# Kernel optimization log

Measured on AMD Instinct MI355X. Metric: run time of the kernel, lower is better.

## Reference

```python
import jax, jax.numpy as jnp
import numpy as np

B, OBS, GENC, H, C, NF = 16384, 512, 216, 1024, 64, 8
IN = GENC + OBS + OBS  # use_state=True: [graph, state, next_state]


def setup_inputs() -> dict:
    key = jax.random.key(0)
    ks = jax.random.split(key, 9)
    graph = jax.random.randint(ks[0], (B, GENC), 0, 2).astype(jnp.float32)
    state = jax.random.normal(ks[1], (B, OBS), dtype=jnp.float32)
    next_state = jax.random.normal(ks[2], (B, OBS), dtype=jnp.float32)
    W1 = jax.random.normal(ks[3], (NF, IN, H), dtype=jnp.float32) * 0.02
    b1 = jnp.zeros((NF, H), dtype=jnp.float32)
    W2 = jax.random.normal(ks[4], (NF, H, H), dtype=jnp.float32) * 0.02
    b2 = jnp.zeros((NF, H), dtype=jnp.float32)
    W3 = jax.random.normal(ks[5], (NF, H, C), dtype=jnp.float32) * 0.02
    b3 = jnp.zeros((NF, C), dtype=jnp.float32)
    return {"graph": graph, "state": state, "next_state": next_state,
            "W1": W1, "b1": b1, "W2": W2, "b2": b2, "W3": W3, "b3": b3}


def reference(graph, state, next_state, W1, b1, W2, b2, W3, b3):
    # wide_diayn forward: concat input, run per-factor MLP on rows where
    # graph[:, i] == 1, later factors overwrite earlier; unmatched rows -> 0.
    x = jnp.concatenate([graph, state, next_state], axis=-1)  # [B, IN]
    nf = W1.shape[0]
    mask = graph[:, :nf] == 1.0  # [B, F] per-factor indicator
    h = jax.nn.relu(jnp.einsum('bi,fih->bfh', x, W1) + b1[None, :, :])
    h = jax.nn.relu(jnp.einsum('bfh,fhg->bfg', h, W2) + b2[None, :, :])
    out_all = jnp.einsum('bfg,fgc->bfc', h, W3) + b3[None, :, :]  # [B, F, C]
    rev_first = jnp.argmax(mask[:, ::-1].astype(jnp.int32), axis=1)
    last_idx = (nf - 1) - rev_first  # [B]
    sel = jnp.take_along_axis(out_all, last_idx[:, None, None], axis=1)[:, 0, :]
    any_active = mask.any(axis=1)
    return jnp.where(any_active[:, None], sel, jnp.zeros_like(sel))
```

## Files before the change

kernel.cpp:

```cpp
#include <hip/hip_runtime.h>

#define BB   16384
#define GENC 216
#define OBS  512
#define NH   1024
#define NC   64
#define NFAC 8
#define NIN  1240
#define KP1  1280
#define MTILES 136

typedef __attribute__((ext_vector_type(4))) float f32x4;
typedef __attribute__((ext_vector_type(8))) short short8;
typedef __attribute__((ext_vector_type(4))) short short4v;

__device__ __forceinline__ unsigned short f2bf(float f) {
  union { float f; unsigned u; } x; x.f = f;
  unsigned r = x.u + 0x7fffu + ((x.u >> 16) & 1u);
  return (unsigned short)(r >> 16);
}

__device__ __forceinline__ void gl_lds16(const unsigned short* g, unsigned short* l) {
  __builtin_amdgcn_global_load_lds(
      (const __attribute__((address_space(1))) void*)g,
      (__attribute__((address_space(3))) void*)l, 16, 0, 0);
}

__device__ __forceinline__ int xcd_chunk(int gid, int nwg) {
  int q = nwg >> 3, r = nwg & 7, x = gid & 7, p = gid >> 3;
  return (x < r ? x * (q + 1) : r * (q + 1) + (x - r) * q) + p;
}

__global__ void bucket_kernel(const float* __restrict__ graph,
                              int* __restrict__ cnt, int* __restrict__ rowlist) {
  __shared__ int lcnt[NFAC];
  __shared__ int lbase[NFAC];
  int tid = threadIdx.x;
  if (tid < NFAC) lcnt[tid] = 0;
  __syncthreads();
  int b = blockIdx.x * 256 + tid;
  const float* g = graph + (size_t)b * GENC;
  float4 g0 = *(const float4*)g;
  float4 g1 = *(const float4*)(g + 4);
  int f = -1;
  if (g0.x == 1.f) f = 0;
  if (g0.y == 1.f) f = 1;
  if (g0.z == 1.f) f = 2;
  if (g0.w == 1.f) f = 3;
  if (g1.x == 1.f) f = 4;
  if (g1.y == 1.f) f = 5;
  if (g1.z == 1.f) f = 6;
  if (g1.w == 1.f) f = 7;
  int li = 0;
  if (f >= 0) li = atomicAdd(&lcnt[f], 1);
  __syncthreads();
  if (tid < NFAC) lbase[tid] = lcnt[tid] ? atomicAdd(&cnt[tid], lcnt[tid]) : 0;
  __syncthreads();
  if (f >= 0) rowlist[f * BB + lbase[f] + li] = b;
}

__global__ void gather_x(const float* __restrict__ graph,
                         const float* __restrict__ state,
                         const float* __restrict__ nexts,
                         const int* __restrict__ cnt,
                         const int* __restrict__ rowlist,
                         unsigned short* __restrict__ xg) {
  int w = threadIdx.x >> 6, lane = threadIdx.x & 63;
  int pos = blockIdx.x * 4 + w;
  int f = -1, loc = 0, acc = 0;
#pragma unroll
  for (int i = 0; i < NFAC; ++i) {
    int c = cnt[i];
    if (f < 0 && pos < acc + c) { f = i; loc = pos - acc; }
    acc += c;
  }
  if (f < 0) return;
  int b = rowlist[f * BB + loc];
  unsigned short* dst = xg + (size_t)pos * KP1;
#pragma unroll
  for (int it = 0; it < 5; ++it) {
    int c = it * 64 + lane;
    float4 v;
    if (c < 54)       v = *(const float4*)(graph + (size_t)b * GENC + c * 4);
    else if (c < 182) v = *(const float4*)(state + (size_t)b * OBS + (c - 54) * 4);
    else if (c < 310) v = *(const float4*)(nexts + (size_t)b * OBS + (c - 182) * 4);
    else              v = make_float4(0.f, 0.f, 0.f, 0.f);
    short4v s;
    s[0] = (short)f2bf(v.x); s[1] = (short)f2bf(v.y);
    s[2] = (short)f2bf(v.z); s[3] = (short)f2bf(v.w);
    *(short4v*)(dst + c * 4) = s;
  }
}

__global__ void transpose_all(const float* __restrict__ W1,
                              const float* __restrict__ W2,
                              const float* __restrict__ W3,
                              unsigned short* __restrict__ w1t,
                              unsigned short* __restrict__ w2t,
                              unsigned short* __restrict__ w3t) {
  __shared__ unsigned short tile[64][65];
  int z = blockIdx.z;
  const float* src; unsigned short* dst; int K, N, KPad;
  if (z < 8)        { src = W1 + (size_t)z * NIN * NH;       dst = w1t + (size_t)z * NH * KP1; K = NIN; N = NH; KPad = KP1; }
  else if (z < 16)  { src = W2 + (size_t)(z - 8) * NH * NH;  dst = w2t + (size_t)(z - 8) * NH * NH; K = NH; N = NH; KPad = NH; }
  else              { src = W3 + (size_t)(z - 16) * NH * NC; dst = w3t + (size_t)(z - 16) * NC * NH; K = NH; N = NC; KPad = NH; }
  int k0 = blockIdx.y * 64, n0 = blockIdx.x * 64;
  if (k0 >= KPad || n0 >= N) return;
  int tr = threadIdx.x >> 6, tc = threadIdx.x & 63;
#pragma unroll
  for (int i = 0; i < 16; ++i) {
    int r = i * 4 + tr;
    int k = k0 + r;
    float v = (k < K) ? src[(size_t)k * N + n0 + tc] : 0.0f;
    tile[r][tc] = f2bf(v);
  }
  __syncthreads();
  int kp = threadIdx.x & 31, nb = threadIdx.x >> 5;
#pragma unroll
  for (int i = 0; i < 8; ++i) {
    int n = i * 8 + nb;
    union { short2 s2; unsigned u; } v;
    v.s2.x = (short)tile[kp * 2][n];
    v.s2.y = (short)tile[kp * 2 + 1][n];
    *(unsigned*)(dst + (size_t)(n0 + n) * KPad + k0 + kp * 2) = v.u;
  }
}

template <int LAYER>
__launch_bounds__(256, 2)
__global__ void mlp_gemm(const unsigned short* __restrict__ Abase,
                         const unsigned short* __restrict__ Wt,
                         const float* __restrict__ bias,
                         unsigned short* __restrict__ Hout,
                         float* __restrict__ Out,
                         const int* __restrict__ cnt,
                         const int* __restrict__ rowlist) {
  constexpr int N  = (LAYER == 3) ? NC : NH;
  constexpr int K  = (LAYER == 1) ? KP1 : NH;
  constexpr int BM = 128;
  constexpr int BN = (LAYER == 3) ? 64 : 128;
  constexpr int NB = (LAYER == 3) ? 1 : (NH / 128);
  constexpr int NKT = K / 64;
  constexpr int MF = (LAYER == 3) ? 2 : 4;
  constexpr int BI = (LAYER == 3) ? 2 : 4;

  const int wg = xcd_chunk(blockIdx.x, MTILES * NB);
  const int ty = wg / NB;
  const int n0 = (wg % NB) * BN;

  int f = -1, m0 = 0, goff = 0, cntf = 0;
  {
    int acc = 0, off = 0;
#pragma unroll
    for (int i = 0; i < NFAC; ++i) {
      int c = cnt[i];
      int t = (c + BM - 1) >> 7;
      if (f < 0 && ty < acc + t) { f = i; m0 = (ty - acc) * BM; goff = off; cntf = c; }
      acc += t; off += c;
    }
  }
  if (f < 0) return;

  __shared__ unsigned short As[2][BM * 64];
  __shared__ unsigned short Bs[2][BN * 64];

  const int tid = threadIdx.x;
  const int wid = tid >> 6, lane = tid & 63;
  const int wm = (LAYER == 3) ? wid : (wid >> 1);
  const int wn = (LAYER == 3) ? 0 : (wid & 1);

  const int rl = lane >> 3;
  const int chs = (lane & 7) ^ rl;
  const unsigned short* pA[4];
  const unsigned short* pB[BI];
  {
    const unsigned short* Aorg = Abase + (size_t)(goff + m0) * K;
    const unsigned short* Borg = Wt + (size_t)f * N * K + (size_t)n0 * K;
#pragma unroll
    for (int i = 0; i < 4; ++i)
      pA[i] = Aorg + (size_t)(wid * 32 + i * 8 + rl) * K + chs * 8;
#pragma unroll
    for (int i = 0; i < BI; ++i)
      pB[i] = Borg + (size_t)(wid * (8 * BI) + i * 8 + rl) * K + chs * 8;
  }

  f32x4 acc[MF][4];
#pragma unroll
  for (int a = 0; a < MF; ++a)
#pragma unroll
    for (int b = 0; b < 4; ++b) acc[a][b] = (f32x4){0.f, 0.f, 0.f, 0.f};

  auto stage = [&](int buf) {
#pragma unroll
    for (int i = 0; i < 4; ++i) {
      gl_lds16(pA[i], &As[buf][(wid * 32 + i * 8) * 64]);
      pA[i] += 64;
    }
#pragma unroll
    for (int i = 0; i < BI; ++i) {
      gl_lds16(pB[i], &Bs[buf][(wid * (8 * BI) + i * 8) * 64]);
      pB[i] += 64;
    }
  };

  auto compute = [&](int buf) {
#pragma unroll
    for (int ks = 0; ks < 2; ++ks) {
      const int kc8 = ks * 4 + (lane >> 4);
      short8 av[MF], bv[4];
#pragma unroll
      for (int mf = 0; mf < MF; ++mf) {
        int row = wm * (MF * 16) + mf * 16 + (lane & 15);
        av[mf] = *(const short8*)(&As[buf][0] + row * 64 + ((kc8 ^ (row & 7)) << 3));
      }
#pragma unroll
      for (int nf = 0; nf < 4; ++nf) {
        int col = wn * 64 + nf * 16 + (lane & 15);
        bv[nf] = *(const short8*)(&Bs[buf][0] + col * 64 + ((kc8 ^ (col & 7)) << 3));
      }
      __builtin_amdgcn_s_setprio(1);
#pragma unroll
      for (int mf = 0; mf < MF; ++mf)
#pragma unroll
        for (int nf = 0; nf < 4; ++nf)
          acc[mf][nf] = __builtin_amdgcn_mfma_f32_16x16x32_bf16(
              av[mf], bv[nf], acc[mf][nf], 0, 0, 0);
      __builtin_amdgcn_s_setprio(0);
    }
  };

  stage(0);
  stage(1);
#pragma unroll 1
  for (int kt = 0; kt < NKT; ++kt) {
    if (kt < NKT - 1) {
      if constexpr (LAYER == 3)
        asm volatile("s_waitcnt vmcnt(6)" ::: "memory");
      else
        asm volatile("s_waitcnt vmcnt(8)" ::: "memory");
    } else {
      asm volatile("s_waitcnt vmcnt(0)" ::: "memory");
    }
    __builtin_amdgcn_sched_barrier(0);
    __builtin_amdgcn_s_barrier();
    __builtin_amdgcn_sched_barrier(0);
    compute(kt & 1);
    __builtin_amdgcn_sched_barrier(0);
    __builtin_amdgcn_s_barrier();
    __builtin_amdgcn_sched_barrier(0);
    if (kt + 2 < NKT) stage(kt & 1);
  }

  if (LAYER == 3) {
    const float* bs = bias + f * NC;
#pragma unroll
    for (int nf = 0; nf < 4; ++nf) {
      int col = nf * 16 + (lane & 15);
      float bv = bs[col];
#pragma unroll
      for (int mf = 0; mf < MF; ++mf) {
        int rbase = wm * (MF * 16) + mf * 16 + ((lane >> 4) << 2);
#pragma unroll
        for (int i = 0; i < 4; ++i) {
          int pos = m0 + rbase + i;
          if (pos < cntf) {
            int b = rowlist[f * BB + pos];
            Out[(size_t)b * NC + col] = acc[mf][nf][i] + bv;
          }
        }
      }
    }
  } else {
    const float* bs = bias + f * NH;
#pragma unroll
    for (int nf = 0; nf < 4; ++nf) {
      int col = n0 + wn * 64 + nf * 16 + (lane & 15);
      float bv = bs[col];
#pragma unroll
      for (int mf = 0; mf < MF; ++mf) {
        int rbase = wm * (MF * 16) + mf * 16 + ((lane >> 4) << 2);
#pragma unroll
        for (int i = 0; i < 4; ++i) {
          int pos = m0 + rbase + i;
          if (pos < cntf) {
            float v = fmaxf(acc[mf][nf][i] + bv, 0.0f);
            Hout[(size_t)(goff + pos) * NH + col] = f2bf(v);
          }
        }
      }
    }
  }
}

extern "C" void kernel_launch(void* const* d_in, const int* in_sizes, int n_in,
                              void* d_out, int out_size, void* d_ws, size_t ws_size,
                              hipStream_t stream) {
  const float* graph = (const float*)d_in[0];
  const float* state = (const float*)d_in[1];
  const float* nexts = (const float*)d_in[2];
  const float* W1 = (const float*)d_in[3];
  const float* b1 = (const float*)d_in[4];
  const float* W2 = (const float*)d_in[5];
  const float* b2 = (const float*)d_in[6];
  const float* W3 = (const float*)d_in[7];
  const float* b3 = (const float*)d_in[8];
  float* out = (float*)d_out;
  char* ws = (char*)d_ws;

  const size_t ROWCAP = BB + 128;
  const size_t OFF_ROW = 256;
  const size_t OFF_W1T = OFF_ROW + (size_t)NFAC * BB * 4;
  const size_t OFF_W2T = OFF_W1T + (size_t)NFAC * NH * KP1 * 2;
  const size_t OFF_W3T = OFF_W2T + (size_t)NFAC * NH * NH * 2;
  const size_t OFF_H1  = OFF_W3T + (size_t)NFAC * NC * NH * 2;
  const size_t OFF_XG  = OFF_H1 + ROWCAP * NH * 2;

  int* cnt = (int*)ws;
  int* rowlist = (int*)(ws + OFF_ROW);
  unsigned short* w1t = (unsigned short*)(ws + OFF_W1T);
  unsigned short* w2t = (unsigned short*)(ws + OFF_W2T);
  unsigned short* w3t = (unsigned short*)(ws + OFF_W3T);
  unsigned short* h1  = (unsigned short*)(ws + OFF_H1);
  unsigned short* xg  = (unsigned short*)(ws + OFF_XG);
  unsigned short* h2  = xg;

  hipMemsetAsync(cnt, 0, 64, stream);
  hipMemsetAsync(d_out, 0, (size_t)out_size * sizeof(float), stream);

  bucket_kernel<<<BB / 256, 256, 0, stream>>>(graph, cnt, rowlist);
  gather_x<<<BB / 4, 256, 0, stream>>>(graph, state, nexts, cnt, rowlist, xg);
  transpose_all<<<dim3(16, 20, 24), 256, 0, stream>>>(W1, W2, W3, w1t, w2t, w3t);

  mlp_gemm<1><<<MTILES * (NH / 128), 256, 0, stream>>>(
      xg, w1t, b1, h1, nullptr, cnt, rowlist);
  mlp_gemm<2><<<MTILES * (NH / 128), 256, 0, stream>>>(
      h1, w2t, b2, h2, nullptr, cnt, rowlist);
  mlp_gemm<3><<<MTILES, 256, 0, stream>>>(
      h2, w3t, b3, nullptr, out, cnt, rowlist);
}
```

Measured before the change: 254.0 us.

## Use 256x256-tile 512-thread GEMM kernel for first two MLP layers

Adds a new GEMM kernel with 256x256 output tiles, 8 waves, 128KB double-buffered LDS with async global-to-LDS loads, split-phase staging and setprio around MFMA blocks. Layers 1 and 2 now use it, with the grid derived from per-factor row counts rounded up to 256. The larger tile raises arithmetic intensity and operand reuse from LDS, but gives fewer workgroups and more padding waste per factor bucket, plus higher register and LDS pressure. The workspace row cap is enlarged to cover the 256-row padding.

```diff
diff --git a/kernel.cpp b/kernel.cpp
--- a/kernel.cpp
+++ b/kernel.cpp
@@ -9,6 +9,7 @@
 #define NIN  1240
 #define KP1  1280
 #define MTILES 136
+#define MT256  72
 
 typedef __attribute__((ext_vector_type(4))) float f32x4;
 typedef __attribute__((ext_vector_type(8))) short short8;
@@ -127,6 +128,172 @@
 }
 
 template <int LAYER>
+__launch_bounds__(512, 2)
+__global__ void mlp_gemm256(const unsigned short* __restrict__ Abase,
+                            const unsigned short* __restrict__ Wt,
+                            const float* __restrict__ bias,
+                            unsigned short* __restrict__ Hout,
+                            const int* __restrict__ cnt) {
+  constexpr int K  = (LAYER == 1) ? KP1 : NH;
+  constexpr int NT = K / 64;
+  constexpr int NB = NH / 256;
+
+  extern __shared__ unsigned short smem[];
+  unsigned short* As0 = smem;
+  unsigned short* As1 = smem + 16384;
+  unsigned short* Bs0 = smem + 32768;
+  unsigned short* Bs1 = smem + 49152;
+
+  const int wg = xcd_chunk(blockIdx.x, MT256 * NB);
+  const int ty = wg / NB;
+  const int n0 = (wg % NB) * 256;
+
+  int f = -1, m0 = 0, goff = 0, cntf = 0;
+  {
+    int acc = 0, off = 0;
+#pragma unroll
+    for (int i = 0; i < NFAC; ++i) {
+      int c = cnt[i];
+      int t = (c + 255) >> 8;
+      if (f < 0 && ty < acc + t) { f = i; m0 = (ty - acc) * 256; goff = off; cntf = c; }
+      acc += t; off += c;
+    }
+  }
+  if (f < 0) return;
+
+  const int tid = threadIdx.x, wid = tid >> 6, lane = tid & 63;
+  const int wm = wid >> 2, wn = wid & 3;
+
+  const int sr = tid >> 3;
+  const int sc = (tid & 7) ^ (sr & 7);
+  const unsigned short* pu[8];
+  {
+    const unsigned short* Ao = Abase + (size_t)(goff + m0) * K;
+    const unsigned short* Bo = Wt + (size_t)f * NH * K + (size_t)n0 * K;
+#pragma unroll
+    for (int u = 0; u < 4; ++u) pu[u] = Ao + (size_t)(u * 64 + sr) * K + sc * 8;
+#pragma unroll
+    for (int u = 0; u < 4; ++u) pu[4 + u] = Bo + (size_t)(u * 64 + sr) * K + sc * 8;
+  }
+  const int ldst = wid * 512;
+
+  f32x4 acc[8][4];
+#pragma unroll
+  for (int a = 0; a < 8; ++a)
+#pragma unroll
+    for (int b = 0; b < 4; ++b) acc[a][b] = (f32x4){0.f, 0.f, 0.f, 0.f};
+
+  auto stage6 = [&](unsigned short* Ab, unsigned short* Bb) {
+    gl_lds16(pu[0], Ab + 0 * 4096 + ldst); pu[0] += 64;
+    gl_lds16(pu[2], Ab + 2 * 4096 + ldst); pu[2] += 64;
+#pragma unroll
+    for (int u = 0; u < 4; ++u) { gl_lds16(pu[4 + u], Bb + u * 4096 + ldst); pu[4 + u] += 64; }
+  };
+  auto stage2 = [&](unsigned short* Ab) {
+    gl_lds16(pu[1], Ab + 1 * 4096 + ldst); pu[1] += 64;
+    gl_lds16(pu[3], Ab + 3 * 4096 + ldst); pu[3] += 64;
+  };
+
+  short8 bfr[4][2];
+
+  stage6(As0, Bs0);
+  stage2(As0);
+
+#pragma unroll 1
+  for (int t = 0; t < NT; ++t) {
+    unsigned short* Ab = (t & 1) ? As1 : As0;
+    unsigned short* Bb = (t & 1) ? Bs1 : Bs0;
+    unsigned short* An = (t & 1) ? As0 : As1;
+    unsigned short* Bn = (t & 1) ? Bs0 : Bs1;
+
+    asm volatile("s_waitcnt vmcnt(2)" ::: "memory");
+    __builtin_amdgcn_sched_barrier(0);
+    __builtin_amdgcn_s_barrier();
+    __builtin_amdgcn_sched_barrier(0);
+    {
+      short8 afr[4][2];
+#pragma unroll
+      for (int nf = 0; nf < 4; ++nf) {
+        int c = wn * 64 + nf * 16 + (lane & 15);
+#pragma unroll
+        for (int ks = 0; ks < 2; ++ks) {
+          int kc = ks * 4 + (lane >> 4);
+          bfr[nf][ks] = *(const short8*)(Bb + c * 64 + ((kc ^ (c & 7)) << 3));
+        }
+      }
+#pragma unroll
+      for (int mf = 0; mf < 4; ++mf) {
+        int r = wm * 128 + mf * 16 + (lane & 15);
+#pragma unroll
+        for (int ks = 0; ks < 2; ++ks) {
+          int kc = ks * 4 + (lane >> 4);
+          afr[mf][ks] = *(const short8*)(Ab + r * 64 + ((kc ^ (r & 7)) << 3));
+        }
+      }
+      if (t + 1 < NT) stage6(An, Bn);
+      __builtin_amdgcn_s_setprio(1);
+#pragma unroll
+      for (int mf = 0; mf < 4; ++mf)
+#pragma unroll
+        for (int nf = 0; nf < 4; ++nf)
+#pragma unroll
+          for (int ks = 0; ks < 2; ++ks)
+            acc[mf][nf] = __builtin_amdgcn_mfma_f32_16x16x32_bf16(
+                afr[mf][ks], bfr[nf][ks], acc[mf][nf], 0, 0, 0);
+      __builtin_amdgcn_s_setprio(0);
+    }
+
+    if (t + 1 < NT) { asm volatile("s_waitcnt vmcnt(6)" ::: "memory"); }
+    else            { asm volatile("s_waitcnt vmcnt(0)" ::: "memory"); }
+    __builtin_amdgcn_sched_barrier(0);
+    __builtin_amdgcn_s_barrier();
+    __builtin_amdgcn_sched_barrier(0);
+    {
+      short8 afr[4][2];
+#pragma unroll
+      for (int mf = 0; mf < 4; ++mf) {
+        int r = wm * 128 + (mf + 4) * 16 + (lane & 15);
+#pragma unroll
+        for (int ks = 0; ks < 2; ++ks) {
+          int kc = ks * 4 + (lane >> 4);
+          afr[mf][ks] = *(const short8*)(Ab + r * 64 + ((kc ^ (r & 7)) << 3));
+        }
+      }
+      if (t + 1 < NT) stage2(An);
+      __builtin_amdgcn_s_setprio(1);
+#pragma unroll
+      for (int mf = 0; mf < 4; ++mf)
+#pragma unroll
+        for (int nf = 0; nf < 4; ++nf)
+#pragma unroll
+          for (int ks = 0; ks < 2; ++ks)
+            acc[mf + 4][nf] = __builtin_amdgcn_mfma_f32_16x16x32_bf16(
+                afr[mf][ks], bfr[nf][ks], acc[mf + 4][nf], 0, 0, 0);
+      __builtin_amdgcn_s_setprio(0);
+    }
+  }
+
+  const float* bs = bias + f * NH;
+#pragma unroll
+  for (int nf = 0; nf < 4; ++nf) {
+    int col = n0 + wn * 64 + nf * 16 + (lane & 15);
+    float bv = bs[col];
+#pragma unroll
+    for (int mf = 0; mf < 8; ++mf) {
+      int rbase = wm * 128 + mf * 16 + ((lane >> 4) << 2);
+#pragma unroll
+      for (int i = 0; i < 4; ++i) {
+        int pos = m0 + rbase + i;
+        if (pos < cntf) {
+          float v = fmaxf(acc[mf][nf][i] + bv, 0.0f);
+          Hout[(size_t)(goff + pos) * NH + col] = f2bf(v);
+        }
+      }
+    }
+  }
+}
+
+template <int LAYER>
 __launch_bounds__(256, 2)
 __global__ void mlp_gemm(const unsigned short* __restrict__ Abase,
                          const unsigned short* __restrict__ Wt,
@@ -307,7 +474,7 @@
   float* out = (float*)d_out;
   char* ws = (char*)d_ws;
 
-  const size_t ROWCAP = BB + 128;
+  const size_t ROWCAP = BB + 256;
   const size_t OFF_ROW = 256;
   const size_t OFF_W1T = OFF_ROW + (size_t)NFAC * BB * 4;
   const size_t OFF_W2T = OFF_W1T + (size_t)NFAC * NH * KP1 * 2;
@@ -324,6 +491,11 @@
   unsigned short* xg  = (unsigned short*)(ws + OFF_XG);
   unsigned short* h2  = xg;
 
+  hipFuncSetAttribute(reinterpret_cast<const void*>(mlp_gemm256<1>),
+                      hipFuncAttributeMaxDynamicSharedMemorySize, 131072);
+  hipFuncSetAttribute(reinterpret_cast<const void*>(mlp_gemm256<2>),
+                      hipFuncAttributeMaxDynamicSharedMemorySize, 131072);
+
   hipMemsetAsync(cnt, 0, 64, stream);
   hipMemsetAsync(d_out, 0, (size_t)out_size * sizeof(float), stream);
 
@@ -331,10 +503,7 @@
   gather_x<<<BB / 4, 256, 0, stream>>>(graph, state, nexts, cnt, rowlist, xg);
   transpose_all<<<dim3(16, 20, 24), 256, 0, stream>>>(W1, W2, W3, w1t, w2t, w3t);
 
-  mlp_gemm<1><<<MTILES * (NH / 128), 256, 0, stream>>>(
-      xg, w1t, b1, h1, nullptr, cnt, rowlist);
-  mlp_gemm<2><<<MTILES * (NH / 128), 256, 0, stream>>>(
-      h1, w2t, b2, h2, nullptr, cnt, rowlist);
-  mlp_gemm<3><<<MTILES, 256, 0, stream>>>(
-      h2, w3t, b3, nullptr, out, cnt, rowlist);
-}
+  mlp_gemm256<1><<<MT256 * 4, 512, 131072, stream>>>(xg, w1t, b1, h1, cnt);
+  mlp_gemm256<2><<<MT256 * 4, 512, 131072, stream>>>(h1, w2t, b2, h2, cnt);
+  mlp_gemm<3><<<MTILES, 256, 0, stream>>>(h2, w3t, b3, nullptr, out, cnt, rowlist);
+}
```

After: 270.1 us. +6.3%, slower.

## Use 128x256 tiles with 8 waves and triple-buffered LDS for hidden GEMMs

Applied to the files above, without the earlier changes.

Layers 1 and 2 move to a new kernel that computes 128x256 output tiles with 512 threads and three LDS buffers in dynamic shared memory. The next stage's global-to-LDS loads are issued after the fragment reads but before the MFMAs, so copies overlap the math. The wider N tile raises the ratio of MFMA work to loaded data and halves the number of A-tile reloads. The cost is large LDS use (about 144 KB), which likely limits each CU to one workgroup. The output layer is split into its own unchanged kernel.

```diff
diff --git a/kernel.cpp b/kernel.cpp
--- a/kernel.cpp
+++ b/kernel.cpp
@@ -127,26 +127,21 @@
 }
 
 template <int LAYER>
-__launch_bounds__(256, 2)
-__global__ void mlp_gemm(const unsigned short* __restrict__ Abase,
-                         const unsigned short* __restrict__ Wt,
-                         const float* __restrict__ bias,
-                         unsigned short* __restrict__ Hout,
-                         float* __restrict__ Out,
-                         const int* __restrict__ cnt,
-                         const int* __restrict__ rowlist) {
-  constexpr int N  = (LAYER == 3) ? NC : NH;
+__launch_bounds__(512, 2)
+__global__ void mlp_gemm_big(const unsigned short* __restrict__ Abase,
+                             const unsigned short* __restrict__ Wt,
+                             const float* __restrict__ bias,
+                             unsigned short* __restrict__ Hout,
+                             const int* __restrict__ cnt) {
   constexpr int K  = (LAYER == 1) ? KP1 : NH;
-  constexpr int BM = 128;
-  constexpr int BN = (LAYER == 3) ? 64 : 128;
-  constexpr int NB = (LAYER == 3) ? 1 : (NH / 128);
-  constexpr int NKT = K / 64;
-  constexpr int MF = (LAYER == 3) ? 2 : 4;
-  constexpr int BI = (LAYER == 3) ? 2 : 4;
+  constexpr int NT = K / 64;
+  constexpr int NB = NH / 256;
+
+  extern __shared__ unsigned short smem[];
 
   const int wg = xcd_chunk(blockIdx.x, MTILES * NB);
   const int ty = wg / NB;
-  const int n0 = (wg % NB) * BN;
+  const int n0 = (wg % NB) * 256;
 
   int f = -1, m0 = 0, goff = 0, cntf = 0;
   {
@@ -154,39 +149,162 @@
 #pragma unroll
     for (int i = 0; i < NFAC; ++i) {
       int c = cnt[i];
-      int t = (c + BM - 1) >> 7;
-      if (f < 0 && ty < acc + t) { f = i; m0 = (ty - acc) * BM; goff = off; cntf = c; }
+      int t = (c + 127) >> 7;
+      if (f < 0 && ty < acc + t) { f = i; m0 = (ty - acc) * 128; goff = off; cntf = c; }
       acc += t; off += c;
     }
   }
   if (f < 0) return;
 
-  __shared__ unsigned short As[2][BM * 64];
-  __shared__ unsigned short Bs[2][BN * 64];
+  const int tid = threadIdx.x, wid = tid >> 6, lane = tid & 63;
+  const int wm = wid >> 2, wn = wid & 3;
+
+  const int sr = tid >> 3;
+  const int sc = (tid & 7) ^ (sr & 7);
+  const unsigned short* pu[6];
+  {
+    const unsigned short* Ao = Abase + (size_t)(goff + m0) * K;
+    const unsigned short* Bo = Wt + (size_t)f * NH * K + (size_t)n0 * K;
+    pu[0] = Ao + (size_t)sr * K + sc * 8;
+    pu[1] = Ao + (size_t)(64 + sr) * K + sc * 8;
+#pragma unroll
+    for (int u = 0; u < 4; ++u) pu[2 + u] = Bo + (size_t)(u * 64 + sr) * K + sc * 8;
+  }
+  const int dst8 = tid * 8;
+
+  unsigned short* A0 = smem;              unsigned short* B0 = smem + 8192;
+  unsigned short* A1 = smem + 24576;      unsigned short* B1 = A1 + 8192;
+  unsigned short* A2 = smem + 49152;      unsigned short* B2 = A2 + 8192;
+
+  f32x4 acc[4][4];
+#pragma unroll
+  for (int a = 0; a < 4; ++a)
+#pragma unroll
+    for (int b = 0; b < 4; ++b) acc[a][b] = (f32x4){0.f, 0.f, 0.f, 0.f};
+
+  auto stage = [&](unsigned short* Ab, unsigned short* Bb) {
+    gl_lds16(pu[0], Ab + dst8);        pu[0] += 64;
+    gl_lds16(pu[1], Ab + 4096 + dst8); pu[1] += 64;
+#pragma unroll
+    for (int u = 0; u < 4; ++u) { gl_lds16(pu[2 + u], Bb + u * 4096 + dst8); pu[2 + u] += 64; }
+  };
+
+  stage(A0, B0);
+  stage(A1, B1);
+  unsigned short *Ac = A0, *Bc = B0, *An = A1, *Bn = B1, *Af = A2, *Bf = B2;
+
+#pragma unroll 1
+  for (int t = 0; t < NT; ++t) {
+    if (t < NT - 1) { asm volatile("s_waitcnt vmcnt(6)" ::: "memory"); }
+    else            { asm volatile("s_waitcnt vmcnt(0)" ::: "memory"); }
+    __builtin_amdgcn_sched_barrier(0);
+    __builtin_amdgcn_s_barrier();
+    __builtin_amdgcn_sched_barrier(0);
+
+    short8 av[4][2], bv[4][2];
+#pragma unroll
+    for (int nf = 0; nf < 4; ++nf) {
+      int c = wn * 64 + nf * 16 + (lane & 15);
+#pragma unroll
+      for (int ks = 0; ks < 2; ++ks) {
+        int kc = ks * 4 + (lane >> 4);
+        bv[nf][ks] = *(const short8*)(Bc + c * 64 + ((kc ^ (c & 7)) << 3));
+      }
+    }
+#pragma unroll
+    for (int mf = 0; mf < 4; ++mf) {
+      int r = wm * 64 + mf * 16 + (lane & 15);
+#pragma unroll
+      for (int ks = 0; ks < 2; ++ks) {
+        int kc = ks * 4 + (lane >> 4);
+        av[mf][ks] = *(const short8*)(Ac + r * 64 + ((kc ^ (r & 7)) << 3));
+      }
+    }
+    if (t + 2 < NT) stage(Af, Bf);
+    __builtin_amdgcn_s_setprio(1);
+#pragma unroll
+    for (int mf = 0; mf < 4; ++mf)
+#pragma unroll
+      for (int nf = 0; nf < 4; ++nf)
+#pragma unroll
+        for (int ks = 0; ks < 2; ++ks)
+          acc[mf][nf] = __builtin_amdgcn_mfma_f32_16x16x32_bf16(
+              av[mf][ks], bv[nf][ks], acc[mf][nf], 0, 0, 0);
+    __builtin_amdgcn_s_setprio(0);
+    unsigned short* ta = Ac; unsigned short* tb = Bc;
+    Ac = An; Bc = Bn; An = Af; Bn = Bf; Af = ta; Bf = tb;
+  }
+
+  const float* bs = bias + f * NH;
+#pragma unroll
+  for (int nf = 0; nf < 4; ++nf) {
+    int col = n0 + wn * 64 + nf * 16 + (lane & 15);
+    float bvv = bs[col];
+#pragma unroll
+    for (int mf = 0; mf < 4; ++mf) {
+      int rbase = wm * 64 + mf * 16 + ((lane >> 4) << 2);
+#pragma unroll
+      for (int i = 0; i < 4; ++i) {
+        int pos = m0 + rbase + i;
+        if (pos < cntf) {
+          float v = fmaxf(acc[mf][nf][i] + bvv, 0.0f);
+          Hout[(size_t)(goff + pos) * NH + col] = f2bf(v);
+        }
+      }
+    }
+  }
+}
+
+__launch_bounds__(256, 2)
+__global__ void mlp_gemm3(const unsigned short* __restrict__ Abase,
+                          const unsigned short* __restrict__ Wt,
+                          const float* __restrict__ bias,
+                          float* __restrict__ Out,
+                          const int* __restrict__ cnt,
+                          const int* __restrict__ rowlist) {
+  constexpr int K = NH;
+  constexpr int NKT = K / 64;
+
+  const int wg = xcd_chunk(blockIdx.x, MTILES);
+  const int ty = wg;
+
+  int f = -1, m0 = 0, goff = 0, cntf = 0;
+  {
+    int acc = 0, off = 0;
+#pragma unroll
+    for (int i = 0; i < NFAC; ++i) {
+      int c = cnt[i];
+      int t = (c + 127) >> 7;
+      if (f < 0 && ty < acc + t) { f = i; m0 = (ty - acc) * 128; goff = off; cntf = c; }
+      acc += t; off += c;
+    }
+  }
+  if (f < 0) return;
+
+  __shared__ unsigned short As[2][128 * 64];
+  __shared__ unsigned short Bs[2][64 * 64];
 
   const int tid = threadIdx.x;
   const int wid = tid >> 6, lane = tid & 63;
-  const int wm = (LAYER == 3) ? wid : (wid >> 1);
-  const int wn = (LAYER == 3) ? 0 : (wid & 1);
 
   const int rl = lane >> 3;
   const int chs = (lane & 7) ^ rl;
   const unsigned short* pA[4];
-  const unsigned short* pB[BI];
+  const unsigned short* pB[2];
   {
     const unsigned short* Aorg = Abase + (size_t)(goff + m0) * K;
-    const unsigned short* Borg = Wt + (size_t)f * N * K + (size_t)n0 * K;
+    const unsigned short* Borg = Wt + (size_t)f * NC * K;
 #pragma unroll
     for (int i = 0; i < 4; ++i)
       pA[i] = Aorg + (size_t)(wid * 32 + i * 8 + rl) * K + chs * 8;
 #pragma unroll
-    for (int i = 0; i < BI; ++i)
-      pB[i] = Borg + (size_t)(wid * (8 * BI) + i * 8 + rl) * K + chs * 8;
-  }
-
-  f32x4 acc[MF][4];
-#pragma unroll
-  for (int a = 0; a < MF; ++a)
+    for (int i = 0; i < 2; ++i)
+      pB[i] = Borg + (size_t)(wid * 16 + i * 8 + rl) * K + chs * 8;
+  }
+
+  f32x4 acc[2][4];
+#pragma unroll
+  for (int a = 0; a < 2; ++a)
 #pragma unroll
     for (int b = 0; b < 4; ++b) acc[a][b] = (f32x4){0.f, 0.f, 0.f, 0.f};
 
@@ -197,8 +315,8 @@
       pA[i] += 64;
     }
 #pragma unroll
-    for (int i = 0; i < BI; ++i) {
-      gl_lds16(pB[i], &Bs[buf][(wid * (8 * BI) + i * 8) * 64]);
+    for (int i = 0; i < 2; ++i) {
+      gl_lds16(pB[i], &Bs[buf][(wid * 16 + i * 8) * 64]);
       pB[i] += 64;
     }
   };
@@ -207,20 +325,20 @@
 #pragma unroll
     for (int ks = 0; ks < 2; ++ks) {
       const int kc8 = ks * 4 + (lane >> 4);
-      short8 av[MF], bv[4];
-#pragma unroll
-      for (int mf = 0; mf < MF; ++mf) {
-        int row = wm * (MF * 16) + mf * 16 + (lane & 15);
+      short8 av[2], bv[4];
+#pragma unroll
+      for (int mf = 0; mf < 2; ++mf) {
+        int row = wid * 32 + mf * 16 + (lane & 15);
         av[mf] = *(const short8*)(&As[buf][0] + row * 64 + ((kc8 ^ (row & 7)) << 3));
       }
 #pragma unroll
       for (int nf = 0; nf < 4; ++nf) {
-        int col = wn * 64 + nf * 16 + (lane & 15);
+        int col = nf * 16 + (lane & 15);
         bv[nf] = *(const short8*)(&Bs[buf][0] + col * 64 + ((kc8 ^ (col & 7)) << 3));
       }
       __builtin_amdgcn_s_setprio(1);
 #pragma unroll
-      for (int mf = 0; mf < MF; ++mf)
+      for (int mf = 0; mf < 2; ++mf)
 #pragma unroll
         for (int nf = 0; nf < 4; ++nf)
           acc[mf][nf] = __builtin_amdgcn_mfma_f32_16x16x32_bf16(
@@ -233,14 +351,8 @@
   stage(1);
 #pragma unroll 1
   for (int kt = 0; kt < NKT; ++kt) {
-    if (kt < NKT - 1) {
-      if constexpr (LAYER == 3)
-        asm volatile("s_waitcnt vmcnt(6)" ::: "memory");
-      else
-        asm volatile("s_waitcnt vmcnt(8)" ::: "memory");
-    } else {
-      asm volatile("s_waitcnt vmcnt(0)" ::: "memory");
-    }
+    if (kt < NKT - 1) { asm volatile("s_waitcnt vmcnt(6)" ::: "memory"); }
+    else              { asm volatile("s_waitcnt vmcnt(0)" ::: "memory"); }
     __builtin_amdgcn_sched_barrier(0);
     __builtin_amdgcn_s_barrier();
     __builtin_amdgcn_sched_barrier(0);
@@ -251,41 +363,20 @@
     if (kt + 2 < NKT) stage(kt & 1);
   }
 
-  if (LAYER == 3) {
-    const float* bs = bias + f * NC;
-#pragma unroll
-    for (int nf = 0; nf < 4; ++nf) {
-      int col = nf * 16 + (lane & 15);
-      float bv = bs[col];
-#pragma unroll
-      for (int mf = 0; mf < MF; ++mf) {
-        int rbase = wm * (MF * 16) + mf * 16 + ((lane >> 4) << 2);
-#pragma unroll
-        for (int i = 0; i < 4; ++i) {
-          int pos = m0 + rbase + i;
-          if (pos < cntf) {
-            int b = rowlist[f * BB + pos];
-            Out[(size_t)b * NC + col] = acc[mf][nf][i] + bv;
-          }
-        }
-      }
-    }
-  } else {
-    const float* bs = bias + f * NH;
-#pragma unroll
-    for (int nf = 0; nf < 4; ++nf) {
-      int col = n0 + wn * 64 + nf * 16 + (lane & 15);
-      float bv = bs[col];
-#pragma unroll
-      for (int mf = 0; mf < MF; ++mf) {
-        int rbase = wm * (MF * 16) + mf * 16 + ((lane >> 4) << 2);
-#pragma unroll
-        for (int i = 0; i < 4; ++i) {
-          int pos = m0 + rbase + i;
-          if (pos < cntf) {
-            float v = fmaxf(acc[mf][nf][i] + bv, 0.0f);
-            Hout[(size_t)(goff + pos) * NH + col] = f2bf(v);
-          }
+  const float* bs = bias + f * NC;
+#pragma unroll
+  for (int nf = 0; nf < 4; ++nf) {
+    int col = nf * 16 + (lane & 15);
+    float bvv = bs[col];
+#pragma unroll
+    for (int mf = 0; mf < 2; ++mf) {
+      int rbase = wid * 32 + mf * 16 + ((lane >> 4) << 2);
+#pragma unroll
+      for (int i = 0; i < 4; ++i) {
+        int pos = m0 + rbase + i;
+        if (pos < cntf) {
+          int b = rowlist[f * BB + pos];
+          Out[(size_t)b * NC + col] = acc[mf][nf][i] + bvv;
         }
       }
     }
@@ -307,7 +398,7 @@
   float* out = (float*)d_out;
   char* ws = (char*)d_ws;
 
-  const size_t ROWCAP = BB + 128;
+  const size_t ROWCAP = BB + 256;
   const size_t OFF_ROW = 256;
   const size_t OFF_W1T = OFF_ROW + (size_t)NFAC * BB * 4;
   const size_t OFF_W2T = OFF_W1T + (size_t)NFAC * NH * KP1 * 2;
@@ -324,6 +415,11 @@
   unsigned short* xg  = (unsigned short*)(ws + OFF_XG);
   unsigned short* h2  = xg;
 
+  hipFuncSetAttribute(reinterpret_cast<const void*>(mlp_gemm_big<1>),
+                      hipFuncAttributeMaxDynamicSharedMemorySize, 147456);
+  hipFuncSetAttribute(reinterpret_cast<const void*>(mlp_gemm_big<2>),
+                      hipFuncAttributeMaxDynamicSharedMemorySize, 147456);
+
   hipMemsetAsync(cnt, 0, 64, stream);
   hipMemsetAsync(d_out, 0, (size_t)out_size * sizeof(float), stream);
 
@@ -331,10 +427,7 @@
   gather_x<<<BB / 4, 256, 0, stream>>>(graph, state, nexts, cnt, rowlist, xg);
   transpose_all<<<dim3(16, 20, 24), 256, 0, stream>>>(W1, W2, W3, w1t, w2t, w3t);
 
-  mlp_gemm<1><<<MTILES * (NH / 128), 256, 0, stream>>>(
-      xg, w1t, b1, h1, nullptr, cnt, rowlist);
-  mlp_gemm<2><<<MTILES * (NH / 128), 256, 0, stream>>>(
-      h1, w2t, b2, h2, nullptr, cnt, rowlist);
-  mlp_gemm<3><<<MTILES, 256, 0, stream>>>(
-      h2, w3t, b3, nullptr, out, cnt, rowlist);
-}
+  mlp_gemm_big<1><<<MTILES * 4, 512, 147456, stream>>>(xg, w1t, b1, h1, cnt);
+  mlp_gemm_big<2><<<MTILES * 4, 512, 147456, stream>>>(h1, w2t, b2, h2, cnt);
+  mlp_gemm3<<<MTILES, 256, 0, stream>>>(h2, w3t, b3, out, cnt, rowlist);
+}
```

After: 243.2 us. 1.04x faster.
